# Kernel tuning notes

Measured on AMD Instinct MI355X. Metric: run time of the kernel, lower is better.

Reference implementation:

```python
import jax, jax.numpy as jnp
import numpy as np

N = 50000        # n nodes (cells)
C = 1024         # common genes
H = 128          # edge_h_dim
HG = 128         # edge_hidden
E = 1600000      # edges (avg degree 32)
LAYERS = 2       # gnn_layers (unset in original __init__; fixed here)
EPS = 1e-8


def setup_inputs() -> dict:
    key = jax.random.key(0)
    ks = jax.random.split(key, 10)
    x_common = jax.random.normal(ks[0], (N, C), dtype=jnp.float32)
    src = jax.random.randint(ks[1], (E,), 0, N, dtype=jnp.int32)
    dst = jax.random.randint(ks[2], (E,), 0, N, dtype=jnp.int32)
    base_w = jax.random.uniform(ks[3], (E,), dtype=jnp.float32)
    # encoder params: Linear(C,H) -> ReLU -> Linear(H,H) -> ReLU
    W1 = jax.random.normal(ks[4], (C, H), dtype=jnp.float32) * 0.02
    b1 = jnp.zeros((H,), dtype=jnp.float32)
    W2 = jax.random.normal(ks[5], (H, H), dtype=jnp.float32) * 0.1
    b2 = jnp.zeros((H,), dtype=jnp.float32)
    # edge gate params: Linear(2H, HG) -> ReLU -> Linear(HG, 1)
    Wg1 = jax.random.normal(ks[6], (2 * H, HG), dtype=jnp.float32) * 0.1
    bg1 = jnp.zeros((HG,), dtype=jnp.float32)
    Wg2 = jax.random.normal(ks[7], (HG, 1), dtype=jnp.float32) * 0.1
    bg2 = jnp.full((1,), 2.0, dtype=jnp.float32)  # original init: bias=2.0
    # node reliability logits
    rho_raw = jax.random.normal(ks[8], (N,), dtype=jnp.float32) * 0.5
    return dict(x_common=x_common, src=src, dst=dst, base_w=base_w,
                W1=W1, b1=b1, W2=W2, b2=b2,
                Wg1=Wg1, bg1=bg1, Wg2=Wg2, bg2=bg2, rho_raw=rho_raw)


def reference(x_common, src, dst, base_w, W1, b1, W2, b2, Wg1, bg1, Wg2, bg2, rho_raw):
    # enc: [N, C] -> [N, H]
    h = jax.nn.relu(jax.nn.relu(x_common @ W1 + b1) @ W2 + b2)
    rho = jax.nn.sigmoid(rho_raw)                 # [N]
    rr = rho[src] * rho[dst]                      # [E] per-edge reliability factor
    for _ in range(LAYERS):
        h_src = h[src]                            # [E, H] gather
        h_dst = h[dst]                            # [E, H] gather
        z = jnp.concatenate([h_src, h_dst], axis=1)               # [E, 2H]
        gate = jax.nn.sigmoid(jax.nn.relu(z @ Wg1 + bg1) @ Wg2 + bg2)[:, 0]  # [E]
        w = base_w * gate * rr                    # [E]
        m = jax.ops.segment_sum(w[:, None] * h_src, dst, num_segments=N)     # [N, H]
        deg = jax.ops.segment_sum(w, dst, num_segments=N)                    # [N]
        h = m / (deg[:, None] + EPS)
    return h
```

## Files before the change

### kernel.cpp

```cpp
#include <hip/hip_runtime.h>
#include <stdint.h>

#define NN 50000
#define CC 1024
#define HH 128
#define EE 1600000
#define EPSV 1e-8f
#define SCAN_BLKS 196
#define ENC_BLKS 782
#define UV_BLKS 782
#define EDGE_BLKS (EE/256)
#define CONV_BLKS 25000
#define PREP_BLKS 704

typedef __attribute__((ext_vector_type(8))) short bf16x8;
typedef __attribute__((ext_vector_type(4))) float f32x4;
typedef __attribute__((ext_vector_type(2))) float f32x2;

__device__ __forceinline__ unsigned short f32_to_bf16(float f){
  union { float f; uint32_t u; } cv; cv.f = f;
  uint32_t u = cv.u;
  return (unsigned short)((u + 0x7FFFu + ((u >> 16) & 1u)) >> 16);
}
__device__ __forceinline__ float bf16lo_to_f32(uint32_t w){
  union { uint32_t u; float f; } cv; cv.u = w << 16; return cv.f;
}
__device__ __forceinline__ float bf16hi_to_f32(uint32_t w){
  union { uint32_t u; float f; } cv; cv.u = w & 0xFFFF0000u; return cv.f;
}

#define DPP_ADD(x, ctrl) ((x) + __int_as_float(__builtin_amdgcn_update_dpp(0, __float_as_int(x), (ctrl), 0xF, 0xF, true)))

#define GLOAD_LDS16(g, l) __builtin_amdgcn_global_load_lds( \
    (const __attribute__((address_space(1))) uint32_t*)(g), \
    (__attribute__((address_space(3))) uint32_t*)(l), 16, 0, 0)


__global__ __launch_bounds__(256) void k_conv_hist_prep(
    const float* __restrict__ X, unsigned short* __restrict__ Xb,
    const int* __restrict__ src, const int* __restrict__ dst,
    int* __restrict__ counts, int* __restrict__ rank,
    const float* __restrict__ W1, const float* __restrict__ W2,
    const float* __restrict__ Wg1,
    unsigned short* __restrict__ W1T, unsigned short* __restrict__ W2T,
    unsigned short* __restrict__ Wg1T)
{
  const int b = blockIdx.x;
  if(b < EDGE_BLKS){
    int e = b*256 + threadIdx.x;
    if(e < EE) rank[e] = atomicAdd(&counts[dst[e]], 1);
    return;
  }
  if(b < EDGE_BLKS + PREP_BLKS){
    int idx = (b - EDGE_BLKS)*256 + threadIdx.x;
    if(idx < 131072){
      int n = idx >> 10, k = idx & 1023;
      W1T[idx] = f32_to_bf16(W1[k*128 + n]);
    } else if(idx < 131072 + 16384){
      int i = idx - 131072;
      int n = i >> 7, k = i & 127;
      W2T[i] = f32_to_bf16(W2[k*128 + n]);
    } else if(idx < 131072 + 16384 + 32768){
      int i = idx - 131072 - 16384;
      int c = i >> 7, k = i & 127;
      int row = (c < 128) ? k : (128 + k);
      int col = (c < 128) ? c : (c - 128);
      Wg1T[i] = f32_to_bf16(Wg1[row*128 + col]);
    }
    return;
  }
  const size_t i = (((size_t)(b - EDGE_BLKS - PREP_BLKS))*256 + threadIdx.x)*8;
  f32x4 v0 = *(const f32x4*)(X + i);
  f32x4 v1 = *(const f32x4*)(X + i + 4);
  union { bf16x8 v; unsigned short s[8]; } pk;
  #pragma unroll
  for(int j = 0; j < 4; j++){ pk.s[j] = f32_to_bf16(v0[j]); pk.s[4+j] = f32_to_bf16(v1[j]); }
  *(bf16x8*)(Xb + i) = pk.v;
}


__global__ __launch_bounds__(256) void k_scan1(const int* __restrict__ counts,
    int* __restrict__ lexcl, int* __restrict__ bsum){
  __shared__ int buf[256];
  const int t = threadIdx.x, i = blockIdx.x*256 + t;
  int v = (i < NN) ? counts[i] : 0;
  buf[t] = v;
  __syncthreads();
  for(int off = 1; off < 256; off <<= 1){
    int add = (t >= off) ? buf[t-off] : 0;
    __syncthreads();
    buf[t] += add;
    __syncthreads();
  }
  if(i < NN) lexcl[i] = buf[t] - v;
  if(t == 255) bsum[blockIdx.x] = buf[255];
}

__global__ __launch_bounds__(256) void k_scan3(const int* __restrict__ lexcl,
    const int* __restrict__ bsum, int* __restrict__ row_ptr){
  __shared__ int red[256];
  const int t = threadIdx.x, b = blockIdx.x;
  red[t] = (t < b) ? bsum[t] : 0;
  __syncthreads();
  for(int off = 1; off < 256; off <<= 1){
    int add = (t >= off) ? red[t-off] : 0;
    __syncthreads();
    red[t] += add;
    __syncthreads();
  }
  const int bexcl = red[255];
  const int i = b*256 + t;
  if(i < NN) row_ptr[i] = lexcl[i] + bexcl;
  if(i == 0) row_ptr[NN] = EE;
}


__global__ __launch_bounds__(256) void k_enc1_fill(
    const unsigned short* __restrict__ Xb, const unsigned short* __restrict__ W1T,
    const float* __restrict__ b1, unsigned short* __restrict__ h1,
    const int* __restrict__ src, const int* __restrict__ dst,
    const float* __restrict__ base_w, const float* __restrict__ rho_raw,
    const int* __restrict__ row_ptr, const int* __restrict__ rank,
    float2* __restrict__ scp)
{
  __shared__ __attribute__((aligned(16))) unsigned short Ab[2][64*32];
  __shared__ __attribute__((aligned(16))) unsigned short Bf[2][128*32];

  if(blockIdx.x >= ENC_BLKS){
    int e = (blockIdx.x - ENC_BLKS)*256 + threadIdx.x;
    if(e < EE){
      int s = src[e], d = dst[e];
      int p = row_ptr[d] + rank[e];
      float rs = 1.f/(1.f + __expf(-rho_raw[s]));
      float rd = 1.f/(1.f + __expf(-rho_raw[d]));
      scp[p] = make_float2(base_w[e]*rs*rd, __int_as_float(s));
    }
    return;
  }

  const int t = threadIdx.x, w = t >> 6, lane = t & 63;
  const int rowL = lane & 15, kq = lane >> 4;
  const int wm = w >> 1, wn = w & 1;
  const int row0 = blockIdx.x * 64;

  const int a_rl  = w*16 + (lane >> 2);
  const int a_cl  = lane & 3;
  const int akeyW = (a_rl ^ (a_rl >> 2)) & 3;
  int agr = row0 + a_rl; if(agr >= NN) agr = NN-1;
  const unsigned short* a_src = Xb + (size_t)agr*1024 + (a_cl ^ akeyW)*8;
  const int b_rl0 = w*32 + (lane >> 2);
  const int b_cl  = lane & 3;
  const int bkey0 = (b_rl0 ^ (b_rl0 >> 2)) & 3;
  const int bkey1 = ((b_rl0+16) ^ ((b_rl0+16) >> 2)) & 3;
  const unsigned short* b_src0 = W1T + (size_t)b_rl0*1024 + (b_cl ^ bkey0)*8;
  const unsigned short* b_src1 = W1T + (size_t)(b_rl0+16)*1024 + (b_cl ^ bkey1)*8;

  #define STAGE(buf, k0)  do{                                              \
    GLOAD_LDS16(a_src  + (k0), &Ab[buf][(w*16)*32]);                       \
    GLOAD_LDS16(b_src0 + (k0), &Bf[buf][(w*32     )*32]);                  \
    GLOAD_LDS16(b_src1 + (k0), &Bf[buf][(w*32 + 16)*32]);                  \
  }while(0)

  f32x4 acc[2][4] = {};
  const int arow0 = wm*32 + rowL;
  const int keyR  = (rowL ^ (rowL >> 2)) & 3;

  auto COMPUTE = [&](const unsigned short* afb, const unsigned short* bfb){
    bf16x8 af[2];
    #pragma unroll
    for(int mf = 0; mf < 2; mf++)
      af[mf] = *(const bf16x8*)&afb[(arow0 + mf*16)*32 + ((kq ^ keyR) << 3)];
    bf16x8 bfr[4];
    #pragma unroll
    for(int nf = 0; nf < 4; nf++){
      const int br = wn*64 + nf*16 + rowL;
      bfr[nf] = *(const bf16x8*)&bfb[br*32 + ((kq ^ keyR) << 3)];
    }
    #pragma unroll
    for(int mf = 0; mf < 2; mf++)
      #pragma unroll
      for(int nf = 0; nf < 4; nf++)
        acc[mf][nf] = __builtin_amdgcn_mfma_f32_16x16x32_bf16(af[mf], bfr[nf], acc[mf][nf], 0, 0, 0);
  };

  #define STEP(cbuf, sbuf, sk)  do{                                        \
    STAGE(sbuf, (sk)*32);                                                  \
    asm volatile("s_waitcnt vmcnt(3)" ::: "memory");                       \
    __builtin_amdgcn_s_barrier();                                          \
    __builtin_amdgcn_sched_barrier(0);                                     \
    COMPUTE(&Ab[cbuf][0], &Bf[cbuf][0]);                                   \
    __builtin_amdgcn_s_barrier();                                          \
  }while(0)

  STAGE(0, 0);
  for(int tt = 0; tt < 30; tt += 2){
    STEP(0, 1, tt + 1);
    STEP(1, 0, tt + 2);
  }
  STEP(0, 1, 31);
  asm volatile("s_waitcnt vmcnt(0)" ::: "memory");
  __builtin_amdgcn_s_barrier();
  __builtin_amdgcn_sched_barrier(0);
  COMPUTE(&Ab[1][0], &Bf[1][0]);
  #undef STEP
  #undef STAGE

  #pragma unroll
  for(int mf = 0; mf < 2; mf++){
    #pragma unroll
    for(int nf = 0; nf < 4; nf++){
      const int col = wn*64 + nf*16 + rowL;
      const float bv = b1[col];
      #pragma unroll
      for(int r = 0; r < 4; r++){
        const int gr = row0 + wm*32 + mf*16 + kq*4 + r;
        if(gr < NN) h1[(size_t)gr*128 + col] = f32_to_bf16(fmaxf(acc[mf][nf][r] + bv, 0.f));
      }
    }
  }
}


__device__ __forceinline__ void uv_phase2(
    const unsigned short* hs, int row0, int w, int lane,
    const unsigned short* __restrict__ Wg1T, const float* __restrict__ bg1,
    unsigned short* __restrict__ UH, float* __restrict__ Vf)
{
  const int rowL = lane & 15, kq = lane >> 4;
  bf16x8 breg[4][4];
  #pragma unroll
  for(int nt = 0; nt < 4; nt++)
    #pragma unroll
    for(int ks = 0; ks < 4; ks++)
      breg[nt][ks] = *(const bf16x8*)(Wg1T + (size_t)(w*64 + nt*16 + rowL)*128 + ks*32 + kq*8);

  #pragma unroll
  for(int mt = 0; mt < 4; mt++){
    const int r = mt*16 + rowL;
    f32x4 acc[4] = {};
    #pragma unroll
    for(int ks = 0; ks < 4; ks++){
      const int kc = ks*4 + kq;
      bf16x8 a = *(const bf16x8*)&hs[r*128 + ((kc ^ rowL) << 3)];
      #pragma unroll
      for(int nt = 0; nt < 4; nt++)
        acc[nt] = __builtin_amdgcn_mfma_f32_16x16x32_bf16(a, breg[nt][ks], acc[nt], 0, 0, 0);
    }
    #pragma unroll
    for(int nt = 0; nt < 4; nt++){
      const int col = w*64 + nt*16 + rowL;
      #pragma unroll
      for(int rr = 0; rr < 4; rr++){
        const int gr = row0 + mt*16 + kq*4 + rr;
        if(gr < NN){
          if(col < 128) UH[(size_t)gr*256 + col] = f32_to_bf16(acc[nt][rr]);
          else          Vf[(size_t)gr*128 + col - 128] = acc[nt][rr] + bg1[col - 128];
        }
      }
    }
  }
}


__global__ __launch_bounds__(256) void k_uvA(
    const unsigned short* __restrict__ h1, const unsigned short* __restrict__ W2T,
    const float* __restrict__ b2, const unsigned short* __restrict__ Wg1T,
    const float* __restrict__ bg1, unsigned short* __restrict__ UH,
    float* __restrict__ Vf)
{
  __shared__ __attribute__((aligned(16))) unsigned short hs[64*128];
  const int t = threadIdx.x, wave = t >> 6, lane = t & 63;
  const int rowL = lane & 15, kq = lane >> 4;
  const int row0 = blockIdx.x*64;

  int ar = row0 + wave*16 + rowL; if(ar >= NN) ar = NN-1;
  f32x4 acc[8] = {};
  #pragma unroll
  for(int ks = 0; ks < 4; ks++){
    bf16x8 a = *(const bf16x8*)(h1 + (size_t)ar*128 + ks*32 + kq*8);
    #pragma unroll
    for(int nt = 0; nt < 8; nt++){
      bf16x8 b = *(const bf16x8*)(W2T + (nt*16 + rowL)*128 + ks*32 + kq*8);
      acc[nt] = __builtin_amdgcn_mfma_f32_16x16x32_bf16(a, b, acc[nt], 0, 0, 0);
    }
  }
  #pragma unroll
  for(int nt = 0; nt < 8; nt++){
    const int col = nt*16 + rowL;
    const float bv = b2[col];
    #pragma unroll
    for(int r = 0; r < 4; r++){
      const int rw = wave*16 + kq*4 + r;
      const unsigned short hv = f32_to_bf16(fmaxf(acc[nt][r] + bv, 0.f));
      hs[rw*128 + (((col >> 3) ^ (rw & 15)) << 3) + (col & 7)] = hv;
    }
  }
  __syncthreads();
  {
    const int r = t >> 2, gr = row0 + r;
    if(gr < NN){
      #pragma unroll
      for(int j8 = 0; j8 < 4; j8++){
        const int chunk = (t & 3)*4 + j8;
        bf16x8 v = *(const bf16x8*)&hs[r*128 + ((chunk ^ (r & 15)) << 3)];
        *(bf16x8*)&UH[(size_t)gr*256 + 128 + chunk*8] = v;
      }
    }
  }
  uv_phase2(hs, row0, wave, lane, Wg1T, bg1, UH, Vf);
}


__global__ __launch_bounds__(256) void k_uvB(
    const unsigned short* __restrict__ Wg1T, const float* __restrict__ bg1,
    unsigned short* __restrict__ UH, float* __restrict__ Vf)
{
  __shared__ __attribute__((aligned(16))) unsigned short hs[64*128];
  const int t = threadIdx.x, wave = t >> 6, lane = t & 63;
  const int row0 = blockIdx.x*64;

  {
    const int r = t >> 2, gr0 = row0 + r;
    const int gr = (gr0 < NN) ? gr0 : NN-1;
    const unsigned short* p = UH + (size_t)gr*256 + 128 + (t & 3)*32;
    #pragma unroll
    for(int j8 = 0; j8 < 4; j8++){
      bf16x8 v = *(const bf16x8*)(p + j8*8);
      const int chunk = (t & 3)*4 + j8;
      *(bf16x8*)&hs[r*128 + ((chunk ^ (r & 15)) << 3)] = v;
    }
  }
  __syncthreads();
  uv_phase2(hs, row0, wave, lane, Wg1T, bg1, UH, Vf);
}


__global__ __launch_bounds__(256) void k_gate_agg(
    const unsigned short* __restrict__ UH, const float* __restrict__ Vf,
    const int* __restrict__ row_ptr, const float2* __restrict__ scp,
    const float* __restrict__ Wg2, const float* __restrict__ bg2p,
    float* __restrict__ out_f32, unsigned short* __restrict__ uh_out)
{
  __shared__ float2 ws_s[4][64];
  const int wv = threadIdx.x >> 6, lane = threadIdx.x & 63;
  const int gw = blockIdx.x*4 + wv;
  if(gw >= NN) return;
  const int eq = lane >> 4, li = lane & 15;

  f32x4 va = *(const f32x4*)(Vf + (size_t)gw*128 + li*8);
  f32x4 vb = *(const f32x4*)(Vf + (size_t)gw*128 + li*8 + 4);
  f32x4 wa = *(const f32x4*)(Wg2 + li*8);
  f32x4 wb = *(const f32x4*)(Wg2 + li*8 + 4);
  const float vch[8]  = {va[0],va[1],va[2],va[3],vb[0],vb[1],vb[2],vb[3]};
  const float w2ch[8] = {wa[0],wa[1],wa[2],wa[3],wb[0],wb[1],wb[2],wb[3]};
  const float bg2v = bg2p[0];

  const int beg = row_ptr[gw], end = row_ptr[gw+1];
  float a0 = 0.f, a1 = 0.f, wsum = 0.f;

  for(int base = beg; base < end; base += 64){
    const int nb = min(64, end - base);

    float2 sc_c0, sc_c1; bf16x8 u_c0, u_c1;
    {
      const int i0 = (eq     < nb) ? eq     : 0;
      const int i1 = (4 + eq < nb) ? 4 + eq : 0;
      sc_c0 = scp[base + i0]; sc_c1 = scp[base + i1];
      u_c0 = *(const bf16x8*)&UH[(uint32_t)__float_as_int(sc_c0.y)*256u + li*8];
      u_c1 = *(const bf16x8*)&UH[(uint32_t)__float_as_int(sc_c1.y)*256u + li*8];
    }
    for(int q = 0; q < nb; q += 8){
      float2 sc_n0 = sc_c0, sc_n1 = sc_c1; bf16x8 u_n0 = u_c0, u_n1 = u_c1;
      if(q + 8 < nb){
        const int i0 = (q + 8  + eq < nb) ? q + 8  + eq : 0;
        const int i1 = (q + 12 + eq < nb) ? q + 12 + eq : 0;
        sc_n0 = scp[base + i0]; sc_n1 = scp[base + i1];
        u_n0 = *(const bf16x8*)&UH[(uint32_t)__float_as_int(sc_n0.y)*256u + li*8];
        u_n1 = *(const bf16x8*)&UH[(uint32_t)__float_as_int(sc_n1.y)*256u + li*8];
      }
      {
        union { bf16x8 v; uint32_t u32[4]; } uu; uu.v = u_c0;
        float tacc = 0.f;
        #pragma unroll
        for(int p = 0; p < 4; p++){
          const uint32_t w2b = uu.u32[p];
          tacc += fmaxf(bf16lo_to_f32(w2b) + vch[2*p],   0.f) * w2ch[2*p];
          tacc += fmaxf(bf16hi_to_f32(w2b) + vch[2*p+1], 0.f) * w2ch[2*p+1];
        }
        tacc = DPP_ADD(tacc, 0xB1);
        tacc = DPP_ADD(tacc, 0x4E);
        tacc = DPP_ADD(tacc, 0x141);
        tacc = DPP_ADD(tacc, 0x140);
        const float g = 1.f/(1.f + __expf(-(tacc + bg2v)));
        const int idx = q + eq;
        if(li == 0 && idx < nb) ws_s[wv][idx] = make_float2(sc_c0.x*g, sc_c0.y);
      }
      {
        union { bf16x8 v; uint32_t u32[4]; } uu; uu.v = u_c1;
        float tacc = 0.f;
        #pragma unroll
        for(int p = 0; p < 4; p++){
          const uint32_t w2b = uu.u32[p];
          tacc += fmaxf(bf16lo_to_f32(w2b) + vch[2*p],   0.f) * w2ch[2*p];
          tacc += fmaxf(bf16hi_to_f32(w2b) + vch[2*p+1], 0.f) * w2ch[2*p+1];
        }
        tacc = DPP_ADD(tacc, 0xB1);
        tacc = DPP_ADD(tacc, 0x4E);
        tacc = DPP_ADD(tacc, 0x141);
        tacc = DPP_ADD(tacc, 0x140);
        const float g = 1.f/(1.f + __expf(-(tacc + bg2v)));
        const int idx = q + 4 + eq;
        if(li == 0 && idx < nb) ws_s[wv][idx] = make_float2(sc_c1.x*g, sc_c1.y);
      }
      sc_c0 = sc_n0; sc_c1 = sc_n1; u_c0 = u_n0; u_c1 = u_n1;
    }

    #pragma unroll 8
    for(int j = 0; j < nb; j++){
      const float2 p = ws_s[wv][j];
      const float w  = p.x;
      const uint32_t s = (uint32_t)__float_as_int(p.y);
      const uint32_t hw = *(const uint32_t*)&UH[s*256u + 128u + lane*2];
      a0 += w*bf16lo_to_f32(hw);
      a1 += w*bf16hi_to_f32(hw);
      wsum += w;
    }
  }
  const float inv = 1.f/(wsum + EPSV);
  const float r0 = a0*inv, r1 = a1*inv;
  if(uh_out){
    const uint32_t packed = (uint32_t)f32_to_bf16(r0) | ((uint32_t)f32_to_bf16(r1) << 16);
    *(uint32_t*)&uh_out[(size_t)gw*256 + 128 + lane*2] = packed;
  } else {
    const size_t o = (size_t)gw*128 + lane*2;
    *(f32x2*)&out_f32[o] = (f32x2){r0, r1};
  }
}


extern "C" void kernel_launch(void* const* d_in, const int* in_sizes, int n_in,
                              void* d_out, int out_size, void* d_ws, size_t ws_size,
                              hipStream_t stream) {
  (void)in_sizes; (void)n_in; (void)out_size; (void)ws_size;
  const float* X      = (const float*)d_in[0];
  const int*   src    = (const int*)d_in[1];
  const int*   dst    = (const int*)d_in[2];
  const float* base_w = (const float*)d_in[3];
  const float* W1     = (const float*)d_in[4];
  const float* b1     = (const float*)d_in[5];
  const float* W2     = (const float*)d_in[6];
  const float* b2     = (const float*)d_in[7];
  const float* Wg1    = (const float*)d_in[8];
  const float* bg1    = (const float*)d_in[9];
  const float* Wg2    = (const float*)d_in[10];
  const float* bg2    = (const float*)d_in[11];
  const float* rho    = (const float*)d_in[12];

  char* ws = (char*)d_ws;
  size_t off = 0;
  auto alloc = [&](size_t bytes)->char*{ char* p = ws + off; off += (bytes + 255) & ~(size_t)255; return p; };
  unsigned short* W1T      = (unsigned short*)alloc((size_t)1024*128*2);
  unsigned short* W2T      = (unsigned short*)alloc((size_t)128*128*2);
  unsigned short* Wg1T     = (unsigned short*)alloc((size_t)256*128*2);
  int*            rank     = (int*)alloc((size_t)EE*4);
  float2*         scp      = (float2*)alloc((size_t)EE*8);
  int*            row_ptr  = (int*)alloc((size_t)(NN+1)*4);
  int*            counts   = (int*)alloc((size_t)NN*4);
  int*            lexcl    = (int*)alloc((size_t)NN*4);
  int*            bsum     = (int*)alloc((size_t)256*4);
  unsigned short* h1       = (unsigned short*)alloc((size_t)NN*128*2);
  unsigned short* UH_A     = (unsigned short*)alloc((size_t)NN*256*2);
  unsigned short* UH_B     = (unsigned short*)alloc((size_t)NN*256*2);
  float*          Vf       = (float*)alloc((size_t)NN*128*4);
  unsigned short* Xb       = (unsigned short*)alloc((size_t)NN*CC*2);

  hipMemsetAsync(counts, 0, (size_t)NN*4, stream);
  k_conv_hist_prep<<<EDGE_BLKS + PREP_BLKS + CONV_BLKS, 256, 0, stream>>>(
      X, Xb, src, dst, counts, rank, W1, W2, Wg1, W1T, W2T, Wg1T);

  k_scan1<<<SCAN_BLKS, 256, 0, stream>>>(counts, lexcl, bsum);
  k_scan3<<<SCAN_BLKS, 256, 0, stream>>>(lexcl, bsum, row_ptr);

  k_enc1_fill<<<ENC_BLKS + EDGE_BLKS, 256, 0, stream>>>(
      Xb, W1T, b1, h1, src, dst, base_w, rho, row_ptr, rank, scp);

  k_uvA<<<UV_BLKS, 256, 0, stream>>>(h1, W2T, b2, Wg1T, bg1, UH_A, Vf);

  k_gate_agg<<<12500, 256, 0, stream>>>(UH_A, Vf, row_ptr, scp, Wg2, bg2, nullptr, UH_B);
  k_uvB<<<UV_BLKS, 256, 0, stream>>>(Wg1T, bg1, UH_B, Vf);
  k_gate_agg<<<12500, 256, 0, stream>>>(UH_B, Vf, row_ptr, scp, Wg2, bg2, (float*)d_out, nullptr);
}
```

Baseline: 493.8 us.

## Fuse fp32-to-bf16 conversion of X into encoder GEMM and reshuffle fill stage

Removes the separate pass that converts X to a bf16 copy. The encoder GEMM now loads fp32 X tiles straight into LDS and converts them to bf16 in registers before the MFMA. The degree histogram moves into the encoder launch, and the CSR fill moves into the uvA launch. This avoids writing and re-reading about 100MB of Xb, but doubles the A-tile LDS footprint and adds conversion work inside the GEMM inner loop.

```diff
diff --git a/kernel.cpp b/kernel.cpp
--- a/kernel.cpp
+++ b/kernel.cpp
@@ -10,7 +10,6 @@
 #define ENC_BLKS 782
 #define UV_BLKS 782
 #define EDGE_BLKS (EE/256)
-#define CONV_BLKS 25000
 #define PREP_BLKS 704
 
 typedef __attribute__((ext_vector_type(8))) short bf16x8;
@@ -36,46 +35,133 @@
     (__attribute__((address_space(3))) uint32_t*)(l), 16, 0, 0)
 
 
-__global__ __launch_bounds__(256) void k_conv_hist_prep(
-    const float* __restrict__ X, unsigned short* __restrict__ Xb,
-    const int* __restrict__ src, const int* __restrict__ dst,
-    int* __restrict__ counts, int* __restrict__ rank,
+__global__ __launch_bounds__(256) void k_prep_all(
     const float* __restrict__ W1, const float* __restrict__ W2,
     const float* __restrict__ Wg1,
     unsigned short* __restrict__ W1T, unsigned short* __restrict__ W2T,
-    unsigned short* __restrict__ Wg1T)
+    unsigned short* __restrict__ Wg1T){
+  int idx = blockIdx.x*256 + threadIdx.x;
+  if(idx < 131072){
+    int n = idx >> 10, k = idx & 1023;
+    W1T[idx] = f32_to_bf16(W1[k*128 + n]);
+  } else if(idx < 131072 + 16384){
+    int i = idx - 131072;
+    int n = i >> 7, k = i & 127;
+    W2T[i] = f32_to_bf16(W2[k*128 + n]);
+  } else if(idx < 131072 + 16384 + 32768){
+    int i = idx - 131072 - 16384;
+    int c = i >> 7, k = i & 127;
+    int row = (c < 128) ? k : (128 + k);
+    int col = (c < 128) ? c : (c - 128);
+    Wg1T[i] = f32_to_bf16(Wg1[row*128 + col]);
+  }
+}
+
+
+__global__ __launch_bounds__(256) void k_enc1_hist(
+    const float* __restrict__ X, const unsigned short* __restrict__ W1T,
+    const float* __restrict__ b1, unsigned short* __restrict__ h1,
+    const int* __restrict__ dst, int* __restrict__ counts, int* __restrict__ rank)
 {
-  const int b = blockIdx.x;
-  if(b < EDGE_BLKS){
-    int e = b*256 + threadIdx.x;
+  __shared__ __attribute__((aligned(16))) float          Af[2][64*32];
+  __shared__ __attribute__((aligned(16))) unsigned short Bf[2][128*32];
+
+  if(blockIdx.x >= ENC_BLKS){
+    int e = (blockIdx.x - ENC_BLKS)*256 + threadIdx.x;
     if(e < EE) rank[e] = atomicAdd(&counts[dst[e]], 1);
     return;
   }
-  if(b < EDGE_BLKS + PREP_BLKS){
-    int idx = (b - EDGE_BLKS)*256 + threadIdx.x;
-    if(idx < 131072){
-      int n = idx >> 10, k = idx & 1023;
-      W1T[idx] = f32_to_bf16(W1[k*128 + n]);
-    } else if(idx < 131072 + 16384){
-      int i = idx - 131072;
-      int n = i >> 7, k = i & 127;
-      W2T[i] = f32_to_bf16(W2[k*128 + n]);
-    } else if(idx < 131072 + 16384 + 32768){
-      int i = idx - 131072 - 16384;
-      int c = i >> 7, k = i & 127;
-      int row = (c < 128) ? k : (128 + k);
-      int col = (c < 128) ? c : (c - 128);
-      Wg1T[i] = f32_to_bf16(Wg1[row*128 + col]);
-    }
-    return;
-  }
-  const size_t i = (((size_t)(b - EDGE_BLKS - PREP_BLKS))*256 + threadIdx.x)*8;
-  f32x4 v0 = *(const f32x4*)(X + i);
-  f32x4 v1 = *(const f32x4*)(X + i + 4);
-  union { bf16x8 v; unsigned short s[8]; } pk;
+
+  const int t = threadIdx.x, w = t >> 6, lane = t & 63;
+  const int rowL = lane & 15, kq = lane >> 4;
+  const int wm = w >> 1, wn = w & 1;
+  const int row0 = blockIdx.x * 64;
+
+  const int a_rl0 = w*16 + (lane >> 3);
+  const int a_cl  = lane & 7;
+  int agr0 = row0 + a_rl0;     if(agr0 >= NN) agr0 = NN-1;
+  int agr1 = row0 + a_rl0 + 8; if(agr1 >= NN) agr1 = NN-1;
+  const float* a_src0 = X + (size_t)agr0*1024 + (a_cl ^ (a_rl0 & 7))*4;
+  const float* a_src1 = X + (size_t)agr1*1024 + (a_cl ^ ((a_rl0+8) & 7))*4;
+  const int b_rl0 = w*32 + (lane >> 2);
+  const int b_cl  = lane & 3;
+  const int bkey0 = (b_rl0 ^ (b_rl0 >> 2)) & 3;
+  const int bkey1 = ((b_rl0+16) ^ ((b_rl0+16) >> 2)) & 3;
+  const unsigned short* b_src0 = W1T + (size_t)b_rl0*1024 + (b_cl ^ bkey0)*8;
+  const unsigned short* b_src1 = W1T + (size_t)(b_rl0+16)*1024 + (b_cl ^ bkey1)*8;
+
+  #define STAGE(buf, k0)  do{                                              \
+    GLOAD_LDS16(a_src0 + (k0), &Af[buf][(w*16    )*32]);                   \
+    GLOAD_LDS16(a_src1 + (k0), &Af[buf][(w*16 + 8)*32]);                   \
+    GLOAD_LDS16(b_src0 + (k0), &Bf[buf][(w*32     )*32]);                  \
+    GLOAD_LDS16(b_src1 + (k0), &Bf[buf][(w*32 + 16)*32]);                  \
+  }while(0)
+
+  f32x4 acc[2][4] = {};
+  const int arow0 = wm*32 + rowL;
+  const int akey  = rowL & 7;
+  const int bkeyR = (rowL ^ (rowL >> 2)) & 3;
+
+  auto COMPUTE = [&](const float* afb, const unsigned short* bfb){
+    bf16x8 af[2];
+    #pragma unroll
+    for(int mf = 0; mf < 2; mf++){
+      const int ar = arow0 + mf*16;
+      f32x4 x0 = *(const f32x4*)&afb[ar*32 + (((2*kq  ) ^ akey) << 2)];
+      f32x4 x1 = *(const f32x4*)&afb[ar*32 + (((2*kq+1) ^ akey) << 2)];
+      union { bf16x8 v; unsigned short s[8]; } pk;
+      #pragma unroll
+      for(int j = 0; j < 4; j++){ pk.s[j] = f32_to_bf16(x0[j]); pk.s[4+j] = f32_to_bf16(x1[j]); }
+      af[mf] = pk.v;
+    }
+    bf16x8 bfr[4];
+    #pragma unroll
+    for(int nf = 0; nf < 4; nf++){
+      const int br = wn*64 + nf*16 + rowL;
+      bfr[nf] = *(const bf16x8*)&bfb[br*32 + ((kq ^ bkeyR) << 3)];
+    }
+    #pragma unroll
+    for(int mf = 0; mf < 2; mf++)
+      #pragma unroll
+      for(int nf = 0; nf < 4; nf++)
+        acc[mf][nf] = __builtin_amdgcn_mfma_f32_16x16x32_bf16(af[mf], bfr[nf], acc[mf][nf], 0, 0, 0);
+  };
+
+  #define STEP(cbuf, sbuf, sk)  do{                                        \
+    STAGE(sbuf, (sk)*32);                                                  \
+    asm volatile("s_waitcnt vmcnt(4)" ::: "memory");                       \
+    __builtin_amdgcn_s_barrier();                                          \
+    __builtin_amdgcn_sched_barrier(0);                                     \
+    COMPUTE(&Af[cbuf][0], &Bf[cbuf][0]);                                   \
+    __builtin_amdgcn_s_barrier();                                          \
+  }while(0)
+
+  STAGE(0, 0);
+  for(int tt = 0; tt < 30; tt += 2){
+    STEP(0, 1, tt + 1);
+    STEP(1, 0, tt + 2);
+  }
+  STEP(0, 1, 31);
+  asm volatile("s_waitcnt vmcnt(0)" ::: "memory");
+  __builtin_amdgcn_s_barrier();
+  __builtin_amdgcn_sched_barrier(0);
+  COMPUTE(&Af[1][0], &Bf[1][0]);
+  #undef STEP
+  #undef STAGE
+
   #pragma unroll
-  for(int j = 0; j < 4; j++){ pk.s[j] = f32_to_bf16(v0[j]); pk.s[4+j] = f32_to_bf16(v1[j]); }
-  *(bf16x8*)(Xb + i) = pk.v;
+  for(int mf = 0; mf < 2; mf++){
+    #pragma unroll
+    for(int nf = 0; nf < 4; nf++){
+      const int col = wn*64 + nf*16 + rowL;
+      const float bv = b1[col];
+      #pragma unroll
+      for(int r = 0; r < 4; r++){
+        const int gr = row0 + wm*32 + mf*16 + kq*4 + r;
+        if(gr < NN) h1[(size_t)gr*128 + col] = f32_to_bf16(fmaxf(acc[mf][nf][r] + bv, 0.f));
+      }
+    }
+  }
 }
 
 
@@ -115,112 +201,6 @@
 }
 
 
-__global__ __launch_bounds__(256) void k_enc1_fill(
-    const unsigned short* __restrict__ Xb, const unsigned short* __restrict__ W1T,
-    const float* __restrict__ b1, unsigned short* __restrict__ h1,
-    const int* __restrict__ src, const int* __restrict__ dst,
-    const float* __restrict__ base_w, const float* __restrict__ rho_raw,
-    const int* __restrict__ row_ptr, const int* __restrict__ rank,
-    float2* __restrict__ scp)
-{
-  __shared__ __attribute__((aligned(16))) unsigned short Ab[2][64*32];
-  __shared__ __attribute__((aligned(16))) unsigned short Bf[2][128*32];
-
-  if(blockIdx.x >= ENC_BLKS){
-    int e = (blockIdx.x - ENC_BLKS)*256 + threadIdx.x;
-    if(e < EE){
-      int s = src[e], d = dst[e];
-      int p = row_ptr[d] + rank[e];
-      float rs = 1.f/(1.f + __expf(-rho_raw[s]));
-      float rd = 1.f/(1.f + __expf(-rho_raw[d]));
-      scp[p] = make_float2(base_w[e]*rs*rd, __int_as_float(s));
-    }
-    return;
-  }
-
-  const int t = threadIdx.x, w = t >> 6, lane = t & 63;
-  const int rowL = lane & 15, kq = lane >> 4;
-  const int wm = w >> 1, wn = w & 1;
-  const int row0 = blockIdx.x * 64;
-
-  const int a_rl  = w*16 + (lane >> 2);
-  const int a_cl  = lane & 3;
-  const int akeyW = (a_rl ^ (a_rl >> 2)) & 3;
-  int agr = row0 + a_rl; if(agr >= NN) agr = NN-1;
-  const unsigned short* a_src = Xb + (size_t)agr*1024 + (a_cl ^ akeyW)*8;
-  const int b_rl0 = w*32 + (lane >> 2);
-  const int b_cl  = lane & 3;
-  const int bkey0 = (b_rl0 ^ (b_rl0 >> 2)) & 3;
-  const int bkey1 = ((b_rl0+16) ^ ((b_rl0+16) >> 2)) & 3;
-  const unsigned short* b_src0 = W1T + (size_t)b_rl0*1024 + (b_cl ^ bkey0)*8;
-  const unsigned short* b_src1 = W1T + (size_t)(b_rl0+16)*1024 + (b_cl ^ bkey1)*8;
-
-  #define STAGE(buf, k0)  do{                                              \
-    GLOAD_LDS16(a_src  + (k0), &Ab[buf][(w*16)*32]);                       \
-    GLOAD_LDS16(b_src0 + (k0), &Bf[buf][(w*32     )*32]);                  \
-    GLOAD_LDS16(b_src1 + (k0), &Bf[buf][(w*32 + 16)*32]);                  \
-  }while(0)
-
-  f32x4 acc[2][4] = {};
-  const int arow0 = wm*32 + rowL;
-  const int keyR  = (rowL ^ (rowL >> 2)) & 3;
-
-  auto COMPUTE = [&](const unsigned short* afb, const unsigned short* bfb){
-    bf16x8 af[2];
-    #pragma unroll
-    for(int mf = 0; mf < 2; mf++)
-      af[mf] = *(const bf16x8*)&afb[(arow0 + mf*16)*32 + ((kq ^ keyR) << 3)];
-    bf16x8 bfr[4];
-    #pragma unroll
-    for(int nf = 0; nf < 4; nf++){
-      const int br = wn*64 + nf*16 + rowL;
-      bfr[nf] = *(const bf16x8*)&bfb[br*32 + ((kq ^ keyR) << 3)];
-    }
-    #pragma unroll
-    for(int mf = 0; mf < 2; mf++)
-      #pragma unroll
-      for(int nf = 0; nf < 4; nf++)
-        acc[mf][nf] = __builtin_amdgcn_mfma_f32_16x16x32_bf16(af[mf], bfr[nf], acc[mf][nf], 0, 0, 0);
-  };
-
-  #define STEP(cbuf, sbuf, sk)  do{                                        \
-    STAGE(sbuf, (sk)*32);                                                  \
-    asm volatile("s_waitcnt vmcnt(3)" ::: "memory");                       \
-    __builtin_amdgcn_s_barrier();                                          \
-    __builtin_amdgcn_sched_barrier(0);                                     \
-    COMPUTE(&Ab[cbuf][0], &Bf[cbuf][0]);                                   \
-    __builtin_amdgcn_s_barrier();                                          \
-  }while(0)
-
-  STAGE(0, 0);
-  for(int tt = 0; tt < 30; tt += 2){
-    STEP(0, 1, tt + 1);
-    STEP(1, 0, tt + 2);
-  }
-  STEP(0, 1, 31);
-  asm volatile("s_waitcnt vmcnt(0)" ::: "memory");
-  __builtin_amdgcn_s_barrier();
-  __builtin_amdgcn_sched_barrier(0);
-  COMPUTE(&Ab[1][0], &Bf[1][0]);
-  #undef STEP
-  #undef STAGE
-
-  #pragma unroll
-  for(int mf = 0; mf < 2; mf++){
-    #pragma unroll
-    for(int nf = 0; nf < 4; nf++){
-      const int col = wn*64 + nf*16 + rowL;
-      const float bv = b1[col];
-      #pragma unroll
-      for(int r = 0; r < 4; r++){
-        const int gr = row0 + wm*32 + mf*16 + kq*4 + r;
-        if(gr < NN) h1[(size_t)gr*128 + col] = f32_to_bf16(fmaxf(acc[mf][nf][r] + bv, 0.f));
-      }
-    }
-  }
-}
-
-
 __device__ __forceinline__ void uv_phase2(
     const unsigned short* hs, int row0, int w, int lane,
     const unsigned short* __restrict__ Wg1T, const float* __restrict__ bg1,
@@ -262,13 +242,30 @@
 }
 
 
-__global__ __launch_bounds__(256) void k_uvA(
+__global__ __launch_bounds__(256) void k_uvA_fill(
     const unsigned short* __restrict__ h1, const unsigned short* __restrict__ W2T,
     const float* __restrict__ b2, const unsigned short* __restrict__ Wg1T,
     const float* __restrict__ bg1, unsigned short* __restrict__ UH,
-    float* __restrict__ Vf)
+    float* __restrict__ Vf,
+    const int* __restrict__ src, const int* __restrict__ dst,
+    const float* __restrict__ base_w, const float* __restrict__ rho_raw,
+    const int* __restrict__ row_ptr, const int* __restrict__ rank,
+    float2* __restrict__ scp)
 {
   __shared__ __attribute__((aligned(16))) unsigned short hs[64*128];
+
+  if(blockIdx.x >= UV_BLKS){
+    int e = (blockIdx.x - UV_BLKS)*256 + threadIdx.x;
+    if(e < EE){
+      int s = src[e], d = dst[e];
+      int p = row_ptr[d] + rank[e];
+      float rs = 1.f/(1.f + __expf(-rho_raw[s]));
+      float rd = 1.f/(1.f + __expf(-rho_raw[d]));
+      scp[p] = make_float2(base_w[e]*rs*rd, __int_as_float(s));
+    }
+    return;
+  }
+
   const int t = threadIdx.x, wave = t >> 6, lane = t & 63;
   const int rowL = lane & 15, kq = lane >> 4;
   const int row0 = blockIdx.x*64;
@@ -472,19 +469,18 @@
   unsigned short* UH_A     = (unsigned short*)alloc((size_t)NN*256*2);
   unsigned short* UH_B     = (unsigned short*)alloc((size_t)NN*256*2);
   float*          Vf       = (float*)alloc((size_t)NN*128*4);
-  unsigned short* Xb       = (unsigned short*)alloc((size_t)NN*CC*2);
 
   hipMemsetAsync(counts, 0, (size_t)NN*4, stream);
-  k_conv_hist_prep<<<EDGE_BLKS + PREP_BLKS + CONV_BLKS, 256, 0, stream>>>(
-      X, Xb, src, dst, counts, rank, W1, W2, Wg1, W1T, W2T, Wg1T);
+  k_prep_all<<<PREP_BLKS, 256, 0, stream>>>(W1, W2, Wg1, W1T, W2T, Wg1T);
+
+  k_enc1_hist<<<ENC_BLKS + EDGE_BLKS, 256, 0, stream>>>(
+      X, W1T, b1, h1, dst, counts, rank);
 
   k_scan1<<<SCAN_BLKS, 256, 0, stream>>>(counts, lexcl, bsum);
   k_scan3<<<SCAN_BLKS, 256, 0, stream>>>(lexcl, bsum, row_ptr);
 
-  k_enc1_fill<<<ENC_BLKS + EDGE_BLKS, 256, 0, stream>>>(
-      Xb, W1T, b1, h1, src, dst, base_w, rho, row_ptr, rank, scp);
-
-  k_uvA<<<UV_BLKS, 256, 0, stream>>>(h1, W2T, b2, Wg1T, bg1, UH_A, Vf);
+  k_uvA_fill<<<UV_BLKS + EDGE_BLKS, 256, 0, stream>>>(
+      h1, W2T, b2, Wg1T, bg1, UH_A, Vf, src, dst, base_w, rho, row_ptr, rank, scp);
 
   k_gate_agg<<<12500, 256, 0, stream>>>(UH_A, Vf, row_ptr, scp, Wg2, bg2, nullptr, UH_B);
   k_uvB<<<UV_BLKS, 256, 0, stream>>>(Wg1T, bg1, UH_B, Vf);
```

Measured after the change: 444.6 us. 1.11x faster.
